# Performance work log

Measured on AMD Instinct MI355X. Metric: run time of the kernel, lower is better.

The kernel has to match this reference:

```python
import jax, jax.numpy as jnp
import numpy as np

B, N, C, H = 2, 2048, 1024, 16
D = C // H
NEG = -1e9  # keras Softmax large negative for masked positions


def setup_inputs() -> dict:
    key = jax.random.key(0)
    ks = jax.random.split(key, 10)
    s = lambda fan_in: 1.0 / np.sqrt(fan_in)
    return {
        "x": jax.random.normal(ks[0], (B, N, C), jnp.float32),
        "mask": jnp.ones((B, 1, 1, N), jnp.bool_),
        "Wqkv": jax.random.normal(ks[1], (C, 3 * C), jnp.float32) * s(C),
        "bqkv": jnp.zeros((3 * C,), jnp.float32),
        "Wl": jax.random.normal(ks[2], (H, H), jnp.float32) * s(H),
        "bl": jnp.zeros((H,), jnp.float32),
        "Ww": jax.random.normal(ks[3], (H, H), jnp.float32) * s(H),
        "bw": jnp.zeros((H,), jnp.float32),
        "Wp": jax.random.normal(ks[4], (C, C), jnp.float32) * s(C),
        "bp": jnp.zeros((C,), jnp.float32),
    }


def reference(x, mask, Wqkv, bqkv, Wl, bl, Ww, bw, Wp, bp):
    scale = jnp.asarray(D ** -0.5, x.dtype)
    qkv = x @ Wqkv + bqkv                                  # [B,N,3C]
    qkv = qkv.reshape(B, N, 3, H, D).transpose(2, 0, 3, 1, 4)  # [3,B,H,N,D]
    q, k, v = qkv[0] * scale, qkv[1], qkv[2]
    attn = jnp.einsum("bhnd,bhmd->bhnm", q, k)             # [B,H,N,N]
    # pre-softmax talking-heads: mix head axis
    attn = jnp.einsum("bhnm,hg->bgnm", attn, Wl) + bl[None, :, None, None]
    # keras Softmax with boolean mask: add -1e9 where mask is False
    attn = attn + (1.0 - mask.astype(attn.dtype)) * NEG
    attn = jax.nn.softmax(attn, axis=-1)
    # post-softmax talking-heads
    attn = jnp.einsum("bhnm,hg->bgnm", attn, Ww) + bw[None, :, None, None]
    out = jnp.einsum("bhnm,bhmd->bhnd", attn, v)           # [B,H,N,D]
    out = out.transpose(0, 2, 1, 3).reshape(B, N, C)
    return out @ Wp + bp
```

## Files before the change

kernel.cpp:

```cpp
#include <hip/hip_runtime.h>
#include <hip/hip_bf16.h>


typedef __bf16 bf16_t;
typedef __bf16 bf16x8 __attribute__((ext_vector_type(8)));
typedef float f32x4 __attribute__((ext_vector_type(4)));

#define DEV static __device__ __forceinline__

static constexpr float NEGV = -1e9f;

DEV f32x4 mfma16(bf16x8 a, bf16x8 b, f32x4 c) {
  return __builtin_amdgcn_mfma_f32_16x16x32_bf16(a, b, c, 0, 0, 0);
}

DEV bf16x8 zero8() {
  bf16x8 z;
#pragma unroll
  for (int j = 0; j < 8; ++j) z[j] = (bf16_t)0.0f;
  return z;
}

__global__ __launch_bounds__(256) void mask_prep(const unsigned char* __restrict__ raw,
                                                 unsigned char* __restrict__ canon) {
  __shared__ int c0, c12;
  const int tid = threadIdx.x;
  if (tid == 0) { c0 = 0; c12 = 0; }
  __syncthreads();
  int l0 = 0, l12 = 0;
  for (int i = tid; i < 4096; i += 256) {
    unsigned char v = raw[i];
    if (v) {
      int r = i & 3;
      if (r == 0) l0++;
      else if (r < 3) l12++;
    }
  }
  if (l0) atomicAdd(&c0, l0);
  if (l12) atomicAdd(&c12, l12);
  __syncthreads();
  const int mode = (c0 == 0) ? 2 : ((c12 > 0) ? 0 : 1);
  for (int i = tid; i < 4096; i += 256) {
    bool t;
    if (mode == 0)      t = raw[i] != 0;
    else if (mode == 1) t = ((const int*)raw)[i] != 0;
    else                t = ((const float*)raw)[i] != 0.0f;
    canon[i] = t ? 1 : 0;
  }
}

__global__ __launch_bounds__(256) void gemm_kernel(
    const float* __restrict__ Af, const bf16_t* __restrict__ Ab,
    const float* __restrict__ Bw, const float* __restrict__ bias,
    float* __restrict__ outf,
    bf16_t* __restrict__ Qs, bf16_t* __restrict__ Ks, bf16_t* __restrict__ Vt,
    int K, int Nn, int epi) {
  __shared__ bf16_t As[64][40];
  __shared__ bf16_t Bs[64][40];
  const int tid = threadIdx.x;
  const int lane = tid & 63, wid = tid >> 6;
  const int bx = blockIdx.x, by = blockIdx.y;
  const int wr = (wid >> 1) * 32, wc = (wid & 1) * 32;
  const int lr = lane & 15, kq = lane >> 4;

  f32x4 acc[2][2];
#pragma unroll
  for (int i = 0; i < 2; ++i)
#pragma unroll
    for (int j = 0; j < 2; ++j) acc[i][j] = (f32x4){0.f, 0.f, 0.f, 0.f};

  for (int kt = 0; kt < K; kt += 32) {
    {
      const int row = tid >> 2, c8 = (tid & 3) * 8;
      if (epi == 0) {
        const float* p = Af + (size_t)(bx * 64 + row) * K + kt + c8;
        float4 v0 = *(const float4*)p;
        float4 v1 = *(const float4*)(p + 4);
        bf16x8 v;
        v[0] = (bf16_t)v0.x; v[1] = (bf16_t)v0.y; v[2] = (bf16_t)v0.z; v[3] = (bf16_t)v0.w;
        v[4] = (bf16_t)v1.x; v[5] = (bf16_t)v1.y; v[6] = (bf16_t)v1.z; v[7] = (bf16_t)v1.w;
        *(bf16x8*)&As[row][c8] = v;
      } else {
        *(bf16x8*)&As[row][c8] =
            *(const bf16x8*)(Ab + (size_t)(bx * 64 + row) * K + kt + c8);
      }
      const int krow = tid >> 3, n8 = (tid & 7) * 8;
      const float* bp = Bw + (size_t)(kt + krow) * Nn + by * 64 + n8;
      float4 b0 = *(const float4*)bp;
      float4 b1 = *(const float4*)(bp + 4);
      Bs[n8 + 0][krow] = (bf16_t)b0.x; Bs[n8 + 1][krow] = (bf16_t)b0.y;
      Bs[n8 + 2][krow] = (bf16_t)b0.z; Bs[n8 + 3][krow] = (bf16_t)b0.w;
      Bs[n8 + 4][krow] = (bf16_t)b1.x; Bs[n8 + 5][krow] = (bf16_t)b1.y;
      Bs[n8 + 6][krow] = (bf16_t)b1.z; Bs[n8 + 7][krow] = (bf16_t)b1.w;
    }
    __syncthreads();
#pragma unroll
    for (int rt = 0; rt < 2; ++rt) {
      bf16x8 af = *(const bf16x8*)&As[wr + rt * 16 + lr][kq * 8];
#pragma unroll
      for (int ct = 0; ct < 2; ++ct) {
        bf16x8 bf = *(const bf16x8*)&Bs[wc + ct * 16 + lr][kq * 8];
        acc[rt][ct] = mfma16(af, bf, acc[rt][ct]);
      }
    }
    __syncthreads();
  }

#pragma unroll
  for (int rt = 0; rt < 2; ++rt)
#pragma unroll
    for (int ct = 0; ct < 2; ++ct)
#pragma unroll
      for (int r = 0; r < 4; ++r) {
        const int grow = bx * 64 + wr + rt * 16 + kq * 4 + r;
        const int gcol = by * 64 + wc + ct * 16 + lr;
        const float v = acc[rt][ct][r] + bias[gcol];
        if (epi == 0) {
          const int t = gcol >> 10, h = (gcol >> 6) & 15, d = gcol & 63;
          const int b = grow >> 11, n = grow & 2047;
          if (t == 0)
            Qs[(((size_t)b * 16 + h) * 2048 + n) * 64 + d] = (bf16_t)(v * 0.125f);
          else if (t == 1)
            Ks[(((size_t)b * 16 + h) * 2048 + n) * 64 + d] = (bf16_t)v;
          else
            Vt[(((size_t)b * 16 + h) * 64 + d) * 2048 + n] = (bf16_t)v;
        } else {
          outf[(size_t)grow * Nn + gcol] = v;
        }
      }
}

__global__ __launch_bounds__(256) void vsum_kernel(const bf16_t* __restrict__ Vt,
                                                   float* __restrict__ Vsum) {
  const int lane = threadIdx.x & 63, wid = threadIdx.x >> 6;
  const int row = blockIdx.x * 4 + wid;
  const bf16_t* p = Vt + (size_t)row * 2048;
  float s = 0.f;
#pragma unroll
  for (int it = 0; it < 4; ++it) {
    bf16x8 v = *(const bf16x8*)(p + it * 512 + lane * 8);
#pragma unroll
    for (int j = 0; j < 8; ++j) s += (float)v[j];
  }
#pragma unroll
  for (int off = 32; off; off >>= 1) s += __shfl_xor(s, off);
  if (lane == 0) Vsum[row] = s;
}

__global__ __launch_bounds__(256) void attn_pass1(
    const bf16_t* __restrict__ Qs, const bf16_t* __restrict__ Ks,
    const unsigned char* __restrict__ canon,
    const float* __restrict__ Wl, const float* __restrict__ bl,
    float2* __restrict__ pstats) {
  __shared__ bf16_t S[512][24];
  const int tid = threadIdx.x, lane = tid & 63, wid = tid >> 6;
  const int g = lane & 15, kq = lane >> 4;
  const int b = blockIdx.z, n0 = blockIdx.x * 16, mbeg = blockIdx.y * 1024;

  bf16x8 wlf;
#pragma unroll
  for (int j = 0; j < 8; ++j) {
    const int k = kq * 8 + j;
    wlf[j] = (k < 16) ? (bf16_t)Wl[k * 16 + g] : (bf16_t)0.0f;
  }
  const float blg = bl[g];

  bf16x8 qf[4][2];
#pragma unroll
  for (int hh = 0; hh < 4; ++hh)
#pragma unroll
    for (int ks = 0; ks < 2; ++ks)
      qf[hh][ks] = *(const bf16x8*)(Qs + (((size_t)b * 16 + wid * 4 + hh) * 2048 +
                                          n0 + g) * 64 + ks * 32 + kq * 8);

  float run_m[4], run_l[4];
#pragma unroll
  for (int i = 0; i < 4; ++i) { run_m[i] = -1e30f; run_l[i] = 0.f; }

  for (int m0 = mbeg; m0 < mbeg + 1024; m0 += 32) {
#pragma unroll
    for (int hh = 0; hh < 4; ++hh) {
      const int h = wid * 4 + hh;
#pragma unroll
      for (int mt = 0; mt < 2; ++mt) {
        f32x4 a = (f32x4){0.f, 0.f, 0.f, 0.f};
#pragma unroll
        for (int ks = 0; ks < 2; ++ks) {
          bf16x8 kf = *(const bf16x8*)(Ks + (((size_t)b * 16 + h) * 2048 + m0 +
                                             mt * 16 + g) * 64 + ks * 32 + kq * 8);
          a = mfma16(qf[hh][ks], kf, a);
        }
#pragma unroll
        for (int r = 0; r < 4; ++r)
          S[(kq * 4 + r) * 32 + mt * 16 + g][h] = (bf16_t)a[r];
      }
    }
    __syncthreads();
#pragma unroll
    for (int pp = 0; pp < 8; ++pp) {
      const int pg = wid * 8 + pp, nloc = pp >> 1;
      bf16x8 sf = (kq < 2) ? *(const bf16x8*)&S[pg * 16 + g][kq * 8] : zero8();
      f32x4 sp = (f32x4){blg, blg, blg, blg};
      sp = mfma16(sf, wlf, sp);
      const int mb = m0 + (pg & 1) * 16 + kq * 4;
      const uchar4 mk = *(const uchar4*)(canon + b * 2048 + mb);
      if (!mk.x) sp[0] += NEGV;
      if (!mk.y) sp[1] += NEGV;
      if (!mk.z) sp[2] += NEGV;
      if (!mk.w) sp[3] += NEGV;
      float tm = fmaxf(fmaxf(sp[0], sp[1]), fmaxf(sp[2], sp[3]));
      tm = fmaxf(tm, __shfl_xor(tm, 16));
      tm = fmaxf(tm, __shfl_xor(tm, 32));
      const float nm = fmaxf(run_m[nloc], tm);
      float s = expf(sp[0] - nm) + expf(sp[1] - nm) + expf(sp[2] - nm) + expf(sp[3] - nm);
      s += __shfl_xor(s, 16);
      s += __shfl_xor(s, 32);
      run_l[nloc] = run_l[nloc] * expf(run_m[nloc] - nm) + s;
      run_m[nloc] = nm;
    }
    __syncthreads();
  }
  if (kq == 0) {
#pragma unroll
    for (int i = 0; i < 4; ++i) {
      const int n = n0 + wid * 4 + i;
      pstats[(((size_t)b * 16 + g) * 2 + blockIdx.y) * 2048 + n] =
          make_float2(run_m[i], run_l[i]);
    }
  }
}

__global__ __launch_bounds__(256) void stats_merge(const float2* __restrict__ ps,
                                                   float2* __restrict__ fin) {
  const int i = blockIdx.x * 256 + threadIdx.x;
  const int row = i >> 11, n = i & 2047;
  const float2 p0 = ps[((size_t)row * 2 + 0) * 2048 + n];
  const float2 p1 = ps[((size_t)row * 2 + 1) * 2048 + n];
  const float M = fmaxf(p0.x, p1.x);
  const float L = p0.y * expf(p0.x - M) + p1.y * expf(p1.x - M);
  fin[i] = make_float2(M, 1.0f / L);
}

__global__ __launch_bounds__(512) void attn_pass2(
    const bf16_t* __restrict__ Qs, const bf16_t* __restrict__ Ks,
    const bf16_t* __restrict__ Vt, const unsigned char* __restrict__ canon,
    const float* __restrict__ Wl, const float* __restrict__ bl,
    const float* __restrict__ Ww, const float2* __restrict__ fin,
    float* __restrict__ Opart) {
  __shared__ bf16_t S[1024][24];
  __shared__ bf16_t F[16][32][40];
  const int tid = threadIdx.x, lane = tid & 63, wid = tid >> 6;
  const int g = lane & 15, kq = lane >> 4;
  const int b = blockIdx.z, n0 = blockIdx.x * 32, mbeg = blockIdx.y * 1024;

  bf16x8 wlf, wwf;
#pragma unroll
  for (int j = 0; j < 8; ++j) {
    const int k = kq * 8 + j;
    wlf[j] = (k < 16) ? (bf16_t)Wl[k * 16 + g] : (bf16_t)0.0f;
    wwf[j] = (k < 16) ? (bf16_t)Ww[k * 16 + g] : (bf16_t)0.0f;
  }
  const float blg = bl[g];

  bf16x8 qf[2][2][2];
#pragma unroll
  for (int hh = 0; hh < 2; ++hh)
#pragma unroll
    for (int rt = 0; rt < 2; ++rt)
#pragma unroll
      for (int ks = 0; ks < 2; ++ks)
        qf[hh][rt][ks] =
            *(const bf16x8*)(Qs + (((size_t)b * 16 + wid * 2 + hh) * 2048 + n0 +
                                   rt * 16 + g) * 64 + ks * 32 + kq * 8);

  float2 fs[4];
#pragma unroll
  for (int i = 0; i < 4; ++i)
    fs[i] = fin[((size_t)b * 16 + g) * 2048 + n0 + wid * 4 + i];

  f32x4 oacc[2][2][4];
#pragma unroll
  for (int i = 0; i < 2; ++i)
#pragma unroll
    for (int j = 0; j < 2; ++j)
#pragma unroll
      for (int k = 0; k < 4; ++k) oacc[i][j][k] = (f32x4){0.f, 0.f, 0.f, 0.f};

  for (int m0 = mbeg; m0 < mbeg + 1024; m0 += 32) {
#pragma unroll
    for (int hh = 0; hh < 2; ++hh) {
      const int h = wid * 2 + hh;
#pragma unroll
      for (int mt = 0; mt < 2; ++mt) {
        f32x4 a0 = (f32x4){0.f, 0.f, 0.f, 0.f};
        f32x4 a1 = (f32x4){0.f, 0.f, 0.f, 0.f};
#pragma unroll
        for (int ks = 0; ks < 2; ++ks) {
          bf16x8 kf = *(const bf16x8*)(Ks + (((size_t)b * 16 + h) * 2048 + m0 +
                                             mt * 16 + g) * 64 + ks * 32 + kq * 8);
          a0 = mfma16(qf[hh][0][ks], kf, a0);
          a1 = mfma16(qf[hh][1][ks], kf, a1);
        }
#pragma unroll
        for (int r = 0; r < 4; ++r) {
          S[(kq * 4 + r) * 32 + mt * 16 + g][h] = (bf16_t)a0[r];
          S[(16 + kq * 4 + r) * 32 + mt * 16 + g][h] = (bf16_t)a1[r];
        }
      }
    }
    __syncthreads();
#pragma unroll
    for (int pp = 0; pp < 8; ++pp) {
      const int pg = wid * 8 + pp, nloc = pp >> 1;
      bf16x8 sf = (kq < 2) ? *(const bf16x8*)&S[pg * 16 + g][kq * 8] : zero8();
      f32x4 sp = (f32x4){blg, blg, blg, blg};
      sp = mfma16(sf, wlf, sp);
      const int mb = m0 + (pg & 1) * 16 + kq * 4;
      const uchar4 mk = *(const uchar4*)(canon + b * 2048 + mb);
      if (!mk.x) sp[0] += NEGV;
      if (!mk.y) sp[1] += NEGV;
      if (!mk.z) sp[2] += NEGV;
      if (!mk.w) sp[3] += NEGV;
      const float2 f2 = fs[nloc];
#pragma unroll
      for (int r = 0; r < 4; ++r) {
        const float e = expf(sp[r] - f2.x) * f2.y;
        S[pg * 16 + kq * 4 + r][g] = (bf16_t)e;
      }
      asm volatile("s_waitcnt lgkmcnt(0)" ::: "memory");
      bf16x8 ef = (kq < 2) ? *(const bf16x8*)&S[pg * 16 + g][kq * 8] : zero8();
      f32x4 fp = (f32x4){0.f, 0.f, 0.f, 0.f};
      fp = mfma16(ef, wwf, fp);
#pragma unroll
      for (int r = 0; r < 4; ++r)
        F[g][pg >> 1][(pg & 1) * 16 + kq * 4 + r] = (bf16_t)fp[r];
    }
    __syncthreads();
#pragma unroll
    for (int g2h = 0; g2h < 2; ++g2h) {
      const int g2 = wid * 2 + g2h;
      bf16x8 af0 = *(const bf16x8*)&F[g2][g][kq * 8];
      bf16x8 af1 = *(const bf16x8*)&F[g2][16 + g][kq * 8];
#pragma unroll
      for (int dt = 0; dt < 4; ++dt) {
        bf16x8 vf = *(const bf16x8*)(Vt + (((size_t)b * 16 + g2) * 64 + dt * 16 +
                                           g) * 2048 + m0 + kq * 8);
        oacc[g2h][0][dt] = mfma16(af0, vf, oacc[g2h][0][dt]);
        oacc[g2h][1][dt] = mfma16(af1, vf, oacc[g2h][1][dt]);
      }
    }
    __syncthreads();
  }

#pragma unroll
  for (int g2h = 0; g2h < 2; ++g2h)
#pragma unroll
    for (int rt = 0; rt < 2; ++rt)
#pragma unroll
      for (int dt = 0; dt < 4; ++dt)
#pragma unroll
        for (int r = 0; r < 4; ++r) {
          const int nl = rt * 16 + kq * 4 + r;
          const int c = (wid * 2 + g2h) * 64 + dt * 16 + g;
          Opart[(((size_t)b * 2 + blockIdx.y) * 2048 + n0 + nl) * 1024 + c] =
              oacc[g2h][rt][dt][r];
        }
}

__global__ __launch_bounds__(256) void reduce_ao(const float* __restrict__ Opart,
                                                 const float* __restrict__ bw,
                                                 const float* __restrict__ Vsum,
                                                 bf16_t* __restrict__ AO) {
  const size_t i = ((size_t)blockIdx.x * 256 + threadIdx.x) * 4;
  const int c = (int)(i & 1023), n = (int)((i >> 10) & 2047), b = (int)(i >> 21);
  const float4 p0 = *(const float4*)&Opart[(((size_t)b * 2 + 0) * 2048 + n) * 1024 + c];
  const float4 p1 = *(const float4*)&Opart[(((size_t)b * 2 + 1) * 2048 + n) * 1024 + c];
  float vv[4] = {p0.x + p1.x, p0.y + p1.y, p0.z + p1.z, p0.w + p1.w};
#pragma unroll
  for (int j = 0; j < 4; ++j) {
    const int cj = c + j, g2 = cj >> 6, d = cj & 63;
    AO[i + j] = (bf16_t)(vv[j] + bw[g2] * Vsum[((size_t)b * 16 + g2) * 64 + d]);
  }
}

extern "C" void kernel_launch(void* const* d_in, const int* in_sizes, int n_in,
                              void* d_out, int out_size, void* d_ws, size_t ws_size,
                              hipStream_t stream) {
  const float* x = (const float*)d_in[0];
  const unsigned char* mask = (const unsigned char*)d_in[1];
  const float* Wqkv = (const float*)d_in[2];
  const float* bqkv = (const float*)d_in[3];
  const float* Wl = (const float*)d_in[4];
  const float* bl = (const float*)d_in[5];
  const float* Ww = (const float*)d_in[6];
  const float* bw = (const float*)d_in[7];
  const float* Wp = (const float*)d_in[8];
  const float* bp = (const float*)d_in[9];
  float* out = (float*)d_out;

  char* w = (char*)d_ws;
  auto alloc = [&](size_t bytes) {
    char* p = w;
    w += (bytes + 255) & ~(size_t)255;
    return p;
  };
  bf16_t* Qs = (bf16_t*)alloc((size_t)2 * 16 * 2048 * 64 * 2);
  bf16_t* Ks = (bf16_t*)alloc((size_t)2 * 16 * 2048 * 64 * 2);
  bf16_t* Vt = (bf16_t*)alloc((size_t)2 * 16 * 2048 * 64 * 2);
  bf16_t* AO = (bf16_t*)alloc((size_t)4096 * 1024 * 2);
  float* Opart = (float*)alloc((size_t)4 * 2048 * 1024 * 4);
  float2* pstats = (float2*)alloc((size_t)2 * 16 * 2 * 2048 * 8);
  float2* fstats = (float2*)alloc((size_t)2 * 16 * 2048 * 8);
  float* Vsum = (float*)alloc((size_t)2048 * 4);
  unsigned char* canon = (unsigned char*)alloc(4096);

  mask_prep<<<dim3(1), dim3(256), 0, stream>>>(mask, canon);
  gemm_kernel<<<dim3(64, 48), dim3(256), 0, stream>>>(
      x, (const bf16_t*)nullptr, Wqkv, bqkv, nullptr, Qs, Ks, Vt, 1024, 3072, 0);
  vsum_kernel<<<dim3(512), dim3(256), 0, stream>>>(Vt, Vsum);
  attn_pass1<<<dim3(128, 2, 2), dim3(256), 0, stream>>>(Qs, Ks, canon, Wl, bl, pstats);
  stats_merge<<<dim3(256), dim3(256), 0, stream>>>(pstats, fstats);
  attn_pass2<<<dim3(64, 2, 2), dim3(512), 0, stream>>>(Qs, Ks, Vt, canon, Wl, bl, Ww,
                                                       fstats, Opart);
  reduce_ao<<<dim3(4096), dim3(256), 0, stream>>>(Opart, bw, Vsum, AO);
  gemm_kernel<<<dim3(64, 16), dim3(256), 0, stream>>>(
      (const float*)nullptr, AO, Wp, bp, out, nullptr, nullptr, nullptr, 1024, 1024, 1);
}
```

Measured before the change: 694.7 us.

## Restructure attention passes with packed swizzled LDS, smaller tiles and more waves

Both attention passes now use 512 threads, each wave handling 2 heads, with launch bounds requesting 4 blocks per CU. Pass2 moves to 16-row query tiles and twice as many blocks. Score tiles are stored in LDS as packed bf16 pairs with XOR swizzles to avoid bank conflicts. The softmax stats layout is transposed to [b, split, n, head] so pass2 can read them with vector loads. Pass2 computes the transposed head-mix MFMA, uses fast __expf, and drops the trailing barrier. The goal is higher occupancy and fewer LDS conflicts and barriers, at the cost of reloading K fragments per smaller tile and a riskier synchronisation scheme.

```diff
diff --git a/kernel.cpp b/kernel.cpp
--- a/kernel.cpp
+++ b/kernel.cpp
@@ -20,6 +20,14 @@
   for (int j = 0; j < 8; ++j) z[j] = (bf16_t)0.0f;
   return z;
 }
+
+DEV uint32_t pkbf(float lo, float hi) {
+  union { bf16_t f; unsigned short s; } a, b;
+  a.f = (bf16_t)lo; b.f = (bf16_t)hi;
+  return (uint32_t)a.s | ((uint32_t)b.s << 16);
+}
+
+union U84 { uint32_t u[4]; bf16x8 v; };
 
 __global__ __launch_bounds__(256) void mask_prep(const unsigned char* __restrict__ raw,
                                                  unsigned char* __restrict__ canon) {
@@ -147,15 +155,16 @@
   if (lane == 0) Vsum[row] = s;
 }
 
-__global__ __launch_bounds__(256) void attn_pass1(
+__global__ __launch_bounds__(512, 4) void attn_pass1(
     const bf16_t* __restrict__ Qs, const bf16_t* __restrict__ Ks,
     const unsigned char* __restrict__ canon,
     const float* __restrict__ Wl, const float* __restrict__ bl,
     float2* __restrict__ pstats) {
-  __shared__ bf16_t S[512][24];
+  __shared__ uint32_t SE[512 * 10];
   const int tid = threadIdx.x, lane = tid & 63, wid = tid >> 6;
   const int g = lane & 15, kq = lane >> 4;
   const int b = blockIdx.z, n0 = blockIdx.x * 16, mbeg = blockIdx.y * 1024;
+  const int h0 = wid * 2;
 
   bf16x8 wlf;
 #pragma unroll
@@ -165,45 +174,47 @@
   }
   const float blg = bl[g];
 
-  bf16x8 qf[4][2];
-#pragma unroll
-  for (int hh = 0; hh < 4; ++hh)
+  bf16x8 qf[2][2];
+#pragma unroll
+  for (int hh = 0; hh < 2; ++hh)
 #pragma unroll
     for (int ks = 0; ks < 2; ++ks)
-      qf[hh][ks] = *(const bf16x8*)(Qs + (((size_t)b * 16 + wid * 4 + hh) * 2048 +
+      qf[hh][ks] = *(const bf16x8*)(Qs + (((size_t)b * 16 + h0 + hh) * 2048 +
                                           n0 + g) * 64 + ks * 32 + kq * 8);
 
-  float run_m[4], run_l[4];
-#pragma unroll
-  for (int i = 0; i < 4; ++i) { run_m[i] = -1e30f; run_l[i] = 0.f; }
+  float run_m[2] = {-3e38f, -3e38f}, run_l[2] = {0.f, 0.f};
 
   for (int m0 = mbeg; m0 < mbeg + 1024; m0 += 32) {
 #pragma unroll
-    for (int hh = 0; hh < 4; ++hh) {
-      const int h = wid * 4 + hh;
-#pragma unroll
-      for (int mt = 0; mt < 2; ++mt) {
-        f32x4 a = (f32x4){0.f, 0.f, 0.f, 0.f};
-#pragma unroll
-        for (int ks = 0; ks < 2; ++ks) {
-          bf16x8 kf = *(const bf16x8*)(Ks + (((size_t)b * 16 + h) * 2048 + m0 +
-                                             mt * 16 + g) * 64 + ks * 32 + kq * 8);
-          a = mfma16(qf[hh][ks], kf, a);
-        }
-#pragma unroll
-        for (int r = 0; r < 4; ++r)
-          S[(kq * 4 + r) * 32 + mt * 16 + g][h] = (bf16_t)a[r];
-      }
-    }
-    __syncthreads();
-#pragma unroll
-    for (int pp = 0; pp < 8; ++pp) {
-      const int pg = wid * 8 + pp, nloc = pp >> 1;
-      bf16x8 sf = (kq < 2) ? *(const bf16x8*)&S[pg * 16 + g][kq * 8] : zero8();
-      f32x4 sp = (f32x4){blg, blg, blg, blg};
-      sp = mfma16(sf, wlf, sp);
-      const int mb = m0 + (pg & 1) * 16 + kq * 4;
-      const uchar4 mk = *(const uchar4*)(canon + b * 2048 + mb);
+    for (int mt = 0; mt < 2; ++mt) {
+      f32x4 a[2];
+#pragma unroll
+      for (int hh = 0; hh < 2; ++hh) {
+        const bf16_t* kp = Ks + (((size_t)b * 16 + h0 + hh) * 2048 + m0 +
+                                 mt * 16 + g) * 64 + kq * 8;
+        a[hh] = mfma16(qf[hh][0], *(const bf16x8*)kp, (f32x4){0.f, 0.f, 0.f, 0.f});
+        a[hh] = mfma16(qf[hh][1], *(const bf16x8*)(kp + 32), a[hh]);
+      }
+#pragma unroll
+      for (int r = 0; r < 4; ++r) {
+        const int p = (kq * 4 + r) * 32 + mt * 16 + g;
+        SE[p * 10 + (wid ^ (kq & 1))] = pkbf(a[0][r], a[1][r]);
+      }
+    }
+    __syncthreads();
+#pragma unroll
+    for (int pp = 0; pp < 4; ++pp) {
+      const int pg = wid * 4 + pp, nl = pp >> 1, mt = pg & 1;
+      const int prow = pg * 16 + g, bp = (prow >> 7) & 1;
+      bf16x8 sf;
+      if (kq < 2) {
+        U84 t;
+#pragma unroll
+        for (int i = 0; i < 4; ++i) t.u[i] = SE[prow * 10 + ((kq * 4 + i) ^ bp)];
+        sf = t.v;
+      } else sf = zero8();
+      f32x4 sp = mfma16(sf, wlf, (f32x4){blg, blg, blg, blg});
+      const uchar4 mk = *(const uchar4*)(canon + b * 2048 + m0 + mt * 16 + kq * 4);
       if (!mk.x) sp[0] += NEGV;
       if (!mk.y) sp[1] += NEGV;
       if (!mk.z) sp[2] += NEGV;
@@ -211,20 +222,21 @@
       float tm = fmaxf(fmaxf(sp[0], sp[1]), fmaxf(sp[2], sp[3]));
       tm = fmaxf(tm, __shfl_xor(tm, 16));
       tm = fmaxf(tm, __shfl_xor(tm, 32));
-      const float nm = fmaxf(run_m[nloc], tm);
-      float s = expf(sp[0] - nm) + expf(sp[1] - nm) + expf(sp[2] - nm) + expf(sp[3] - nm);
+      const float nm = fmaxf(run_m[nl], tm);
+      float s = __expf(sp[0] - nm) + __expf(sp[1] - nm) +
+                __expf(sp[2] - nm) + __expf(sp[3] - nm);
       s += __shfl_xor(s, 16);
       s += __shfl_xor(s, 32);
-      run_l[nloc] = run_l[nloc] * expf(run_m[nloc] - nm) + s;
-      run_m[nloc] = nm;
+      run_l[nl] = run_l[nl] * __expf(run_m[nl] - nm) + s;
+      run_m[nl] = nm;
     }
     __syncthreads();
   }
   if (kq == 0) {
 #pragma unroll
-    for (int i = 0; i < 4; ++i) {
-      const int n = n0 + wid * 4 + i;
-      pstats[(((size_t)b * 16 + g) * 2 + blockIdx.y) * 2048 + n] =
+    for (int i = 0; i < 2; ++i) {
+      const int n = n0 + wid * 2 + i;
+      pstats[(((size_t)b * 2 + blockIdx.y) * 2048 + n) * 16 + g] =
           make_float2(run_m[i], run_l[i]);
     }
   }
@@ -233,138 +245,138 @@
 __global__ __launch_bounds__(256) void stats_merge(const float2* __restrict__ ps,
                                                    float2* __restrict__ fin) {
   const int i = blockIdx.x * 256 + threadIdx.x;
-  const int row = i >> 11, n = i & 2047;
-  const float2 p0 = ps[((size_t)row * 2 + 0) * 2048 + n];
-  const float2 p1 = ps[((size_t)row * 2 + 1) * 2048 + n];
+  const int b = i >> 15, rest = i & 32767;
+  const float2 p0 = ps[((size_t)b * 2 + 0) * 32768 + rest];
+  const float2 p1 = ps[((size_t)b * 2 + 1) * 32768 + rest];
   const float M = fmaxf(p0.x, p1.x);
-  const float L = p0.y * expf(p0.x - M) + p1.y * expf(p1.x - M);
+  const float L = p0.y * __expf(p0.x - M) + p1.y * __expf(p1.x - M);
   fin[i] = make_float2(M, 1.0f / L);
 }
 
-__global__ __launch_bounds__(512) void attn_pass2(
+__global__ __launch_bounds__(512, 4) void attn_pass2(
     const bf16_t* __restrict__ Qs, const bf16_t* __restrict__ Ks,
     const bf16_t* __restrict__ Vt, const unsigned char* __restrict__ canon,
     const float* __restrict__ Wl, const float* __restrict__ bl,
-    const float* __restrict__ Ww, const float2* __restrict__ fin,
+    const float* __restrict__ Ww, const float2* __restrict__ fin2,
     float* __restrict__ Opart) {
-  __shared__ bf16_t S[1024][24];
-  __shared__ bf16_t F[16][32][40];
+  __shared__ uint32_t SE[512 * 10];
+  __shared__ uint32_t Fw[16 * 324];
   const int tid = threadIdx.x, lane = tid & 63, wid = tid >> 6;
   const int g = lane & 15, kq = lane >> 4;
-  const int b = blockIdx.z, n0 = blockIdx.x * 32, mbeg = blockIdx.y * 1024;
-
-  bf16x8 wlf, wwf;
+  const int b = blockIdx.z, n0 = blockIdx.x * 16, mbeg = blockIdx.y * 1024;
+  const int h0 = wid * 2;
+
+  bf16x8 wlf, wwt;
 #pragma unroll
   for (int j = 0; j < 8; ++j) {
     const int k = kq * 8 + j;
     wlf[j] = (k < 16) ? (bf16_t)Wl[k * 16 + g] : (bf16_t)0.0f;
-    wwf[j] = (k < 16) ? (bf16_t)Ww[k * 16 + g] : (bf16_t)0.0f;
-  }
-  const float blg = bl[g];
-
-  bf16x8 qf[2][2][2];
+    wwt[j] = (k < 16) ? (bf16_t)Ww[k * 16 + g] : (bf16_t)0.0f;
+  }
+  f32x4 blv;
+#pragma unroll
+  for (int r = 0; r < 4; ++r) blv[r] = bl[kq * 4 + r];
+
+  bf16x8 qf[2][2];
 #pragma unroll
   for (int hh = 0; hh < 2; ++hh)
 #pragma unroll
-    for (int rt = 0; rt < 2; ++rt)
-#pragma unroll
-      for (int ks = 0; ks < 2; ++ks)
-        qf[hh][rt][ks] =
-            *(const bf16x8*)(Qs + (((size_t)b * 16 + wid * 2 + hh) * 2048 + n0 +
-                                   rt * 16 + g) * 64 + ks * 32 + kq * 8);
-
-  float2 fs[4];
-#pragma unroll
-  for (int i = 0; i < 4; ++i)
-    fs[i] = fin[((size_t)b * 16 + g) * 2048 + n0 + wid * 4 + i];
-
-  f32x4 oacc[2][2][4];
+    for (int ks = 0; ks < 2; ++ks)
+      qf[hh][ks] = *(const bf16x8*)(Qs + (((size_t)b * 16 + h0 + hh) * 2048 +
+                                          n0 + g) * 64 + ks * 32 + kq * 8);
+
+  f32x4 oacc[2][4];
 #pragma unroll
   for (int i = 0; i < 2; ++i)
 #pragma unroll
-    for (int j = 0; j < 2; ++j)
-#pragma unroll
-      for (int k = 0; k < 4; ++k) oacc[i][j][k] = (f32x4){0.f, 0.f, 0.f, 0.f};
+    for (int j = 0; j < 4; ++j) oacc[i][j] = (f32x4){0.f, 0.f, 0.f, 0.f};
 
   for (int m0 = mbeg; m0 < mbeg + 1024; m0 += 32) {
 #pragma unroll
-    for (int hh = 0; hh < 2; ++hh) {
-      const int h = wid * 2 + hh;
-#pragma unroll
-      for (int mt = 0; mt < 2; ++mt) {
-        f32x4 a0 = (f32x4){0.f, 0.f, 0.f, 0.f};
-        f32x4 a1 = (f32x4){0.f, 0.f, 0.f, 0.f};
-#pragma unroll
-        for (int ks = 0; ks < 2; ++ks) {
-          bf16x8 kf = *(const bf16x8*)(Ks + (((size_t)b * 16 + h) * 2048 + m0 +
-                                             mt * 16 + g) * 64 + ks * 32 + kq * 8);
-          a0 = mfma16(qf[hh][0][ks], kf, a0);
-          a1 = mfma16(qf[hh][1][ks], kf, a1);
-        }
-#pragma unroll
-        for (int r = 0; r < 4; ++r) {
-          S[(kq * 4 + r) * 32 + mt * 16 + g][h] = (bf16_t)a0[r];
-          S[(16 + kq * 4 + r) * 32 + mt * 16 + g][h] = (bf16_t)a1[r];
-        }
-      }
-    }
-    __syncthreads();
-#pragma unroll
-    for (int pp = 0; pp < 8; ++pp) {
-      const int pg = wid * 8 + pp, nloc = pp >> 1;
-      bf16x8 sf = (kq < 2) ? *(const bf16x8*)&S[pg * 16 + g][kq * 8] : zero8();
-      f32x4 sp = (f32x4){blg, blg, blg, blg};
-      sp = mfma16(sf, wlf, sp);
-      const int mb = m0 + (pg & 1) * 16 + kq * 4;
-      const uchar4 mk = *(const uchar4*)(canon + b * 2048 + mb);
-      if (!mk.x) sp[0] += NEGV;
-      if (!mk.y) sp[1] += NEGV;
-      if (!mk.z) sp[2] += NEGV;
-      if (!mk.w) sp[3] += NEGV;
-      const float2 f2 = fs[nloc];
+    for (int mt = 0; mt < 2; ++mt) {
+      f32x4 a[2];
+#pragma unroll
+      for (int hh = 0; hh < 2; ++hh) {
+        const bf16_t* kp = Ks + (((size_t)b * 16 + h0 + hh) * 2048 + m0 +
+                                 mt * 16 + g) * 64 + kq * 8;
+        a[hh] = mfma16(qf[hh][0], *(const bf16x8*)kp, (f32x4){0.f, 0.f, 0.f, 0.f});
+        a[hh] = mfma16(qf[hh][1], *(const bf16x8*)(kp + 32), a[hh]);
+      }
 #pragma unroll
       for (int r = 0; r < 4; ++r) {
-        const float e = expf(sp[r] - f2.x) * f2.y;
-        S[pg * 16 + kq * 4 + r][g] = (bf16_t)e;
-      }
+        const int p = (kq * 4 + r) * 32 + mt * 16 + g;
+        SE[p * 10 + (wid ^ (kq & 1))] = pkbf(a[0][r], a[1][r]);
+      }
+    }
+    __syncthreads();
+#pragma unroll
+    for (int pp = 0; pp < 4; ++pp) {
+      const int pg = wid * 4 + pp, nl = pg >> 1, mt = pg & 1;
+      const int prow = pg * 16 + g, bp = (prow >> 7) & 1;
+      bf16x8 sf;
+      if (kq < 2) {
+        U84 t;
+#pragma unroll
+        for (int i = 0; i < 4; ++i) t.u[i] = SE[prow * 10 + ((kq * 4 + i) ^ bp)];
+        sf = t.v;
+      } else sf = zero8();
+      f32x4 sp = mfma16(wlf, sf, blv);
+      if (!canon[b * 2048 + m0 + mt * 16 + g]) {
+        sp[0] += NEGV; sp[1] += NEGV; sp[2] += NEGV; sp[3] += NEGV;
+      }
+      const float4* st = (const float4*)((const float*)fin2 +
+                          (((size_t)b * 2048 + n0 + nl) * 16 + kq * 4) * 2);
+      const float4 s01 = st[0], s23 = st[1];
+      const float e0 = __expf(sp[0] - s01.x) * s01.y;
+      const float e1 = __expf(sp[1] - s01.z) * s01.w;
+      const float e2 = __expf(sp[2] - s23.x) * s23.y;
+      const float e3 = __expf(sp[3] - s23.z) * s23.w;
+      uint2 ew;
+      ew.x = pkbf(e0, e1);
+      ew.y = pkbf(e2, e3);
+      *(uint2*)&SE[prow * 10 + kq * 2] = ew;
       asm volatile("s_waitcnt lgkmcnt(0)" ::: "memory");
-      bf16x8 ef = (kq < 2) ? *(const bf16x8*)&S[pg * 16 + g][kq * 8] : zero8();
-      f32x4 fp = (f32x4){0.f, 0.f, 0.f, 0.f};
-      fp = mfma16(ef, wwf, fp);
+      __builtin_amdgcn_sched_barrier(0);
+      bf16x8 ef;
+      if (kq < 2) {
+        U84 t;
+#pragma unroll
+        for (int i = 0; i < 4; ++i) t.u[i] = SE[prow * 10 + kq * 4 + i];
+        ef = t.v;
+      } else ef = zero8();
+      f32x4 fp = mfma16(wwt, ef, (f32x4){0.f, 0.f, 0.f, 0.f});
+      const int melem = mt * 16 + g;
+      const int wm = (melem >> 1) ^ ((nl & 3) << 2);
 #pragma unroll
       for (int r = 0; r < 4; ++r)
-        F[g][pg >> 1][(pg & 1) * 16 + kq * 4 + r] = (bf16_t)fp[r];
+        ((bf16_t*)Fw)[(((kq * 4 + r) * 324) + nl * 20 + wm) * 2 + (melem & 1)] =
+            (bf16_t)fp[r];
     }
     __syncthreads();
 #pragma unroll
     for (int g2h = 0; g2h < 2; ++g2h) {
-      const int g2 = wid * 2 + g2h;
-      bf16x8 af0 = *(const bf16x8*)&F[g2][g][kq * 8];
-      bf16x8 af1 = *(const bf16x8*)&F[g2][16 + g][kq * 8];
+      const int g2 = h0 + g2h;
+      bf16x8 af = *(const bf16x8*)&Fw[g2 * 324 + g * 20 + ((kq ^ (g & 3)) << 2)];
 #pragma unroll
       for (int dt = 0; dt < 4; ++dt) {
         bf16x8 vf = *(const bf16x8*)(Vt + (((size_t)b * 16 + g2) * 64 + dt * 16 +
                                            g) * 2048 + m0 + kq * 8);
-        oacc[g2h][0][dt] = mfma16(af0, vf, oacc[g2h][0][dt]);
-        oacc[g2h][1][dt] = mfma16(af1, vf, oacc[g2h][1][dt]);
-      }
-    }
-    __syncthreads();
+        oacc[g2h][dt] = mfma16(af, vf, oacc[g2h][dt]);
+      }
+    }
   }
 
 #pragma unroll
   for (int g2h = 0; g2h < 2; ++g2h)
 #pragma unroll
-    for (int rt = 0; rt < 2; ++rt)
-#pragma unroll
-      for (int dt = 0; dt < 4; ++dt)
-#pragma unroll
-        for (int r = 0; r < 4; ++r) {
-          const int nl = rt * 16 + kq * 4 + r;
-          const int c = (wid * 2 + g2h) * 64 + dt * 16 + g;
-          Opart[(((size_t)b * 2 + blockIdx.y) * 2048 + n0 + nl) * 1024 + c] =
-              oacc[g2h][rt][dt][r];
-        }
+    for (int dt = 0; dt < 4; ++dt)
+#pragma unroll
+      for (int r = 0; r < 4; ++r) {
+        const int n = n0 + kq * 4 + r;
+        const int c = (h0 + g2h) * 64 + dt * 16 + g;
+        Opart[(((size_t)b * 2 + blockIdx.y) * 2048 + n) * 1024 + c] =
+            oacc[g2h][dt][r];
+      }
 }
 
 __global__ __launch_bounds__(256) void reduce_ao(const float* __restrict__ Opart,
@@ -409,8 +421,8 @@
   bf16_t* Vt = (bf16_t*)alloc((size_t)2 * 16 * 2048 * 64 * 2);
   bf16_t* AO = (bf16_t*)alloc((size_t)4096 * 1024 * 2);
   float* Opart = (float*)alloc((size_t)4 * 2048 * 1024 * 4);
-  float2* pstats = (float2*)alloc((size_t)2 * 16 * 2 * 2048 * 8);
-  float2* fstats = (float2*)alloc((size_t)2 * 16 * 2048 * 8);
+  float2* pstats = (float2*)alloc((size_t)2 * 2 * 2048 * 16 * 8);
+  float2* fstats = (float2*)alloc((size_t)2 * 2048 * 16 * 8);
   float* Vsum = (float*)alloc((size_t)2048 * 4);
   unsigned char* canon = (unsigned char*)alloc(4096);
 
@@ -418,10 +430,10 @@
   gemm_kernel<<<dim3(64, 48), dim3(256), 0, stream>>>(
       x, (const bf16_t*)nullptr, Wqkv, bqkv, nullptr, Qs, Ks, Vt, 1024, 3072, 0);
   vsum_kernel<<<dim3(512), dim3(256), 0, stream>>>(Vt, Vsum);
-  attn_pass1<<<dim3(128, 2, 2), dim3(256), 0, stream>>>(Qs, Ks, canon, Wl, bl, pstats);
+  attn_pass1<<<dim3(128, 2, 2), dim3(512), 0, stream>>>(Qs, Ks, canon, Wl, bl, pstats);
   stats_merge<<<dim3(256), dim3(256), 0, stream>>>(pstats, fstats);
-  attn_pass2<<<dim3(64, 2, 2), dim3(512), 0, stream>>>(Qs, Ks, Vt, canon, Wl, bl, Ww,
-                                                       fstats, Opart);
+  attn_pass2<<<dim3(128, 2, 2), dim3(512), 0, stream>>>(Qs, Ks, Vt, canon, Wl, bl, Ww,
+                                                        fstats, Opart);
   reduce_ao<<<dim3(4096), dim3(256), 0, stream>>>(Opart, bw, Vsum, AO);
   gemm_kernel<<<dim3(64, 16), dim3(256), 0, stream>>>(
       (const float*)nullptr, AO, Wp, bp, out, nullptr, nullptr, nullptr, 1024, 1024, 1);
```

Result: no change. 683.7 us (-1.6%).
